# Kernel tuning notes

Measured on AMD Instinct MI355X. Metric: run time of the kernel, lower is better.

The kernel has to match this reference:

```python
import jax, jax.numpy as jnp
import numpy as np

NUM_SITES = 64
BOND_DIM = 64
PHYS_DIM = 2
BATCH = 8192
INIT_STD = 0.125  # 1/sqrt(bond_dim)
EPS_AMP = 1e-12
EPS_LOG = 1e-30


def setup_inputs() -> dict:
    key = jax.random.key(0)
    k_cfg, k_l, k_b, k_r = jax.random.split(key, 4)
    configurations = jax.random.randint(k_cfg, (BATCH, NUM_SITES), 0, PHYS_DIM, dtype=jnp.int32)
    left = jax.random.normal(k_l, (PHYS_DIM, BOND_DIM), dtype=jnp.float32) * INIT_STD
    bulk = jax.random.normal(k_b, (NUM_SITES - 2, BOND_DIM, PHYS_DIM, BOND_DIM), dtype=jnp.float32) * INIT_STD
    right = jax.random.normal(k_r, (BOND_DIM, PHYS_DIM), dtype=jnp.float32) * INIT_STD
    return {"configurations": configurations, "left": left, "bulk": bulk, "right": right}


def _psi(configurations, left, bulk, right):
    # configurations: [B, S] int; left: [d, D]; bulk: [S-2, D, d, D]; right: [D, d]
    B = configurations.shape[0]
    env0 = left[configurations[:, 0]]  # [B, D]
    cfg_mid = configurations[:, 1:-1].T  # [S-2, B]

    def step(env, xs):
        site_t, idx = xs  # site_t: [D, d, D], idx: [B]
        D = site_t.shape[0]
        # env @ site (contract left bond), then gather the per-sample physical slice
        tmp = (env @ site_t.reshape(D, -1)).reshape(B, PHYS_DIM, D)  # [B, d, D]
        env = jnp.take_along_axis(tmp, idx[:, None, None], axis=1)[:, 0, :]  # [B, D]
        return env, None

    env, _ = jax.lax.scan(step, env0, (bulk, cfg_mid))
    cols = jnp.take(right, configurations[:, -1], axis=1).T  # [B, D]
    return jnp.sum(env * cols, axis=1)  # [B]


def _log_norm(left, bulk, right):
    env0 = left.T @ left  # [D, D]  (real dtype -> conj trivial)

    def step(carry, site_t):
        env, log_scale = carry
        sm = jnp.transpose(site_t, (1, 0, 2))  # [d, D, D]
        env = jnp.einsum('pdi,de,pej->ij', sm, env, sm)  # sum_p A_p^H env A_p
        scale = jnp.maximum(jnp.max(jnp.abs(env)), EPS_LOG)
        return (env / scale, log_scale + jnp.log(scale)), None

    (env, log_scale), _ = jax.lax.scan(step, (env0, jnp.zeros((), left.dtype)), bulk)
    z = jnp.sum(right * (env @ right))
    return jnp.log(jnp.maximum(z, EPS_LOG)) + log_scale


def reference(configurations, left, bulk, right):
    psi = _psi(configurations, left, bulk, right)
    abs_sq = jnp.maximum(psi * psi, EPS_AMP)
    log_z = _log_norm(left, bulk, right)
    nll = -(jnp.log(abs_sq) - log_z)
    return jnp.mean(nll)
```

## Files before the change

kernel.cpp:

```cpp
#include <hip/hip_runtime.h>
#include <math.h>

#define NBULK 62
#define SB    72

typedef __attribute__((ext_vector_type(8))) short bf8_t;
typedef __attribute__((ext_vector_type(4))) float f4_t;

#define MFMA(a, b, c) __builtin_amdgcn_mfma_f32_16x16x32_bf16((a), (b), (c), 0, 0, 0)

__device__ __forceinline__ unsigned short f2bf(float f) {
    unsigned int u = __float_as_uint(f);
    return (unsigned short)((u + 0x7FFFu + ((u >> 16) & 1u)) >> 16);
}
__device__ __forceinline__ float bf2f(unsigned short h) {
    return __uint_as_float(((unsigned int)h) << 16);
}

__device__ __forceinline__ void gload16(const void* g, void* l) {
    __builtin_amdgcn_global_load_lds(
        (const __attribute__((address_space(1))) unsigned int*)g,
        (__attribute__((address_space(3))) unsigned int*)l, 16, 0, 0);
}

#define WS_E_OFF   1024
#define WS_B_OFF   6144
#define WS_BT_OFF  45056
#define WS_MR_OFF  1060864


extern "C" __global__ __launch_bounds__(256)
void mps_precompute(const float* __restrict__ bulkG,
                    unsigned short* __restrict__ BTg,
                    unsigned short* __restrict__ MRg)
{
    __shared__ unsigned short BTl[8192];
    __shared__ unsigned short MRl[8192];
    const int s = blockIdx.x, tid = threadIdx.x;
    const float4* src = (const float4*)(bulkG + (size_t)s * 8192);
    for (int c = 0; c < 8; ++c) {
        int idx = tid + c * 256;
        float4 v = src[idx];
        int f  = idx * 4;
        int kk = f >> 7;
        int p  = (f >> 6) & 1;
        int j  = f & 63;
        unsigned short b0 = f2bf(v.x), b1 = f2bf(v.y), b2 = f2bf(v.z), b3 = f2bf(v.w);
        int n = p * 64 + kk;
        int off = n * 64 + (((j >> 3) ^ (n & 7)) << 3) + (j & 7);
        MRl[off + 0] = b0; MRl[off + 1] = b1; MRl[off + 2] = b2; MRl[off + 3] = b3;
        unsigned short bb[4] = {b0, b1, b2, b3};
        #pragma unroll
        for (int t2 = 0; t2 < 4; ++t2) {
            int n2 = p * 64 + j + t2;
            BTl[n2 * 64 + (((kk >> 3) ^ (n2 & 7)) << 3) + (kk & 7)] = bb[t2];
        }
    }
    __syncthreads();
    const uint4* bt4 = (const uint4*)BTl;
    const uint4* mr4 = (const uint4*)MRl;
    uint4* btg = (uint4*)(BTg + (size_t)s * 8192);
    uint4* mrg = (uint4*)(MRg + (size_t)s * 8192);
    for (int c = 0; c < 4; ++c) {
        int idx = tid + c * 256;
        btg[idx] = bt4[idx];
        mrg[idx] = mr4[idx];
    }
}

extern "C" __global__ __launch_bounds__(256)
void mps_main(const int* __restrict__ cfgG, const float* __restrict__ leftG,
              const float* __restrict__ rightG, float* __restrict__ wsF,
              const unsigned short* __restrict__ BTg,
              const unsigned short* __restrict__ MRg)
{
    extern __shared__ char smem[];
    unsigned short* smem16 = (unsigned short*)smem;
    const int tid  = threadIdx.x;
    const int bid  = blockIdx.x;
    const int wv   = tid >> 6;
    const int lane = tid & 63;
    const int quad = lane >> 4;
    const int ln   = lane & 15;

    if (bid >= 2) {
        unsigned short* Bb0  = smem16;
        unsigned short* Bb1  = Bb0 + 8192;
        unsigned short* env  = Bb1 + 8192;
        unsigned char*  selT = (unsigned char*)(env + 64 * SB);

        const int s0 = (bid - 2) * 64;
        {
            int m = tid >> 2, part = tid & 3;
            const int* row = cfgG + (size_t)(s0 + m) * 64 + part * 16;
            #pragma unroll
            for (int q = 0; q < 4; ++q) {
                int4 v = *(const int4*)(row + q * 4);
                int cb = part * 16 + q * 4;
                selT[(cb + 0) * 64 + m] = (unsigned char)v.x;
                selT[(cb + 1) * 64 + m] = (unsigned char)v.y;
                selT[(cb + 2) * 64 + m] = (unsigned char)v.z;
                selT[(cb + 3) * 64 + m] = (unsigned char)v.w;
            }
        }
        {
            const char* g0 = (const char*)BTg;
            for (int c = 0; c < 4; ++c) {
                int chunk = wv * 4 + c;
                gload16(g0 + chunk * 1024 + (size_t)lane * 16, (char*)Bb0 + chunk * 1024);
            }
        }
        __syncthreads();

        bf8_t Af[2];
        {
            int sel0 = selT[0 * 64 + wv * 16 + ln];
            const float* lp0 = leftG + sel0 * 64;
            #pragma unroll
            for (int h = 0; h < 2; ++h) {
                float4 a = *(const float4*)(lp0 + h * 32 + quad * 8);
                float4 b = *(const float4*)(lp0 + h * 32 + quad * 8 + 4);
                bf8_t t;
                t[0] = (short)f2bf(a.x); t[1] = (short)f2bf(a.y);
                t[2] = (short)f2bf(a.z); t[3] = (short)f2bf(a.w);
                t[4] = (short)f2bf(b.x); t[5] = (short)f2bf(b.y);
                t[6] = (short)f2bf(b.z); t[7] = (short)f2bf(b.w);
                Af[h] = t;
            }
        }

        for (int t = 0; t < NBULK; ++t) {
            __syncthreads();
            unsigned short* B = (t & 1) ? Bb1 : Bb0;
            if (t + 1 < NBULK) {
                const char* gn = (const char*)(BTg + (size_t)(t + 1) * 8192);
                char* l = (char*)((t & 1) ? Bb0 : Bb1);
                for (int c = 0; c < 4; ++c) {
                    int chunk = wv * 4 + c;
                    gload16(gn + chunk * 1024 + (size_t)lane * 16, l + chunk * 1024);
                }
            }
            bf8_t Bf[2][4][2];
            #pragma unroll
            for (int b2 = 0; b2 < 2; ++b2)
                #pragma unroll
                for (int ct = 0; ct < 4; ++ct) {
                    int row = b2 * 64 + ct * 16 + ln;
                    #pragma unroll
                    for (int h = 0; h < 2; ++h)
                        Bf[b2][ct][h] = *(const bf8_t*)(B + row * 64 + (((h * 4 + quad) ^ (ln & 7)) << 3));
                }
            f4_t acc[2][4];
            #pragma unroll
            for (int b2 = 0; b2 < 2; ++b2)
                #pragma unroll
                for (int ct = 0; ct < 4; ++ct) {
                    f4_t a = {0.f, 0.f, 0.f, 0.f};
                    a = MFMA(Af[0], Bf[b2][ct][0], a);
                    a = MFMA(Af[1], Bf[b2][ct][1], a);
                    acc[b2][ct] = a;
                }
            unsigned int sv = *(const unsigned int*)(selT + (t + 1) * 64 + wv * 16 + quad * 4);
            #pragma unroll
            for (int ct = 0; ct < 4; ++ct)
                #pragma unroll
                for (int r = 0; r < 4; ++r) {
                    float v = ((sv >> (8 * r)) & 1u) ? acc[1][ct][r] : acc[0][ct][r];
                    env[(wv * 16 + quad * 4 + r) * SB + ct * 16 + ln] = f2bf(v);
                }
            Af[0] = *(const bf8_t*)(env + (wv * 16 + ln) * SB + quad * 8);
            Af[1] = *(const bf8_t*)(env + (wv * 16 + ln) * SB + 32 + quad * 8);
        }
        {
            int selL = selT[63 * 64 + wv * 16 + ln];
            bf8_t e0 = *(const bf8_t*)(env + (wv * 16 + ln) * SB + quad * 16);
            bf8_t e1 = *(const bf8_t*)(env + (wv * 16 + ln) * SB + quad * 16 + 8);
            float p = 0.f;
            #pragma unroll
            for (int j = 0; j < 8; ++j)
                p = fmaf(bf2f((unsigned short)e0[j]), rightG[(quad * 16 + j) * 2 + selL], p);
            #pragma unroll
            for (int j = 0; j < 8; ++j)
                p = fmaf(bf2f((unsigned short)e1[j]), rightG[(quad * 16 + 8 + j) * 2 + selL], p);
            p += __shfl_xor(p, 16);
            p += __shfl_xor(p, 32);
            float lp = logf(fmaxf(p * p, 1e-12f));
            lp += __shfl_xor(lp, 1); lp += __shfl_xor(lp, 2);
            lp += __shfl_xor(lp, 4); lp += __shfl_xor(lp, 8);
            if (lane == 0) atomicAdd(&wsF[0], lp);
        }
    } else {
        unsigned short* Ebf = smem16;
        unsigned short* St0 = Ebf + 64 * SB;
        unsigned short* St1 = St0 + 64 * SB;
        unsigned short* Ms0 = St1 + 64 * SB;
        unsigned short* Ms1 = Ms0 + 8192;
        float* wred = (float*)(Ms1 + 8192);

        const bool fwd = (bid == 0);
        const unsigned short* srcbase = fwd ? BTg : MRg;
        {
            int i = tid >> 2, jq = tid & 3;
            for (int jj = 0; jj < 16; ++jj) {
                int j = jq * 16 + jj;
                float v;
                if (fwd) v = leftG[i] * leftG[j] + leftG[64 + i] * leftG[64 + j];
                else     v = rightG[i * 2] * rightG[j * 2] + rightG[i * 2 + 1] * rightG[j * 2 + 1];
                Ebf[i * SB + j] = f2bf(v);
            }
        }
        {
            int st = fwd ? 0 : 61;
            const char* g = (const char*)(srcbase + (size_t)st * 8192);
            for (int c = 0; c < 4; ++c) {
                int chunk = wv * 4 + c;
                gload16(g + chunk * 1024 + (size_t)lane * 16, (char*)Ms0 + chunk * 1024);
            }
        }
        float lsum = 0.f;
        const int p   = wv >> 1;
        const int ntb = (wv & 1) * 2;
        const int mta = (wv >> 1) * 2;
        const int nta = (wv & 1) * 2;
        unsigned short* Stp = p ? St1 : St0;

        for (int k = 0; k < 31; ++k) {
            __syncthreads();
            unsigned short* M = (k & 1) ? Ms1 : Ms0;
            if (k + 1 < 31) {
                int sn = fwd ? (k + 1) : (61 - (k + 1));
                const char* g = (const char*)(srcbase + (size_t)sn * 8192);
                char* l = (char*)((k & 1) ? Ms0 : Ms1);
                for (int c = 0; c < 4; ++c) {
                    int chunk = wv * 4 + c;
                    gload16(g + chunk * 1024 + (size_t)lane * 16, l + chunk * 1024);
                }
            }
            float inv = 1.f;
            if (k > 0) {
                const float* wp = wred + ((k - 1) & 1) * 4;
                float mm = fmaxf(fmaxf(wp[0], wp[1]), fmaxf(wp[2], wp[3]));
                float sc = fmaxf(mm, 1e-30f);
                inv = 1.f / sc;
                if (tid == 0) lsum += logf(sc);
            }
            {
                bf8_t Af2[4][2];
                #pragma unroll
                for (int mt = 0; mt < 4; ++mt)
                    #pragma unroll
                    for (int h = 0; h < 2; ++h)
                        Af2[mt][h] = *(const bf8_t*)(Ebf + (mt * 16 + ln) * SB + h * 32 + quad * 8);
                #pragma unroll
                for (int c = 0; c < 2; ++c) {
                    int nt = ntb + c;
                    int row = p * 64 + nt * 16 + ln;
                    bf8_t B0 = *(const bf8_t*)(M + row * 64 + (((0 + quad) ^ (ln & 7)) << 3));
                    bf8_t B1 = *(const bf8_t*)(M + row * 64 + (((4 + quad) ^ (ln & 7)) << 3));
                    #pragma unroll
                    for (int mt = 0; mt < 4; ++mt) {
                        f4_t a = {0.f, 0.f, 0.f, 0.f};
                        a = MFMA(Af2[mt][0], B0, a);
                        a = MFMA(Af2[mt][1], B1, a);
                        ushort4 pk;
                        pk.x = f2bf(a[0]); pk.y = f2bf(a[1]); pk.z = f2bf(a[2]); pk.w = f2bf(a[3]);
                        *(ushort4*)(Stp + (nt * 16 + ln) * SB + mt * 16 + quad * 4) = pk;
                    }
                }
            }
            __syncthreads();
            {
                bf8_t Aw[2][2][2], Bw[2][2][2];
                #pragma unroll
                for (int pp = 0; pp < 2; ++pp)
                    #pragma unroll
                    for (int mi = 0; mi < 2; ++mi)
                        #pragma unroll
                        for (int h = 0; h < 2; ++h)
                            Aw[pp][mi][h] = *(const bf8_t*)(M + (pp * 64 + (mta + mi) * 16 + ln) * 64
                                                              + (((h * 4 + quad) ^ (ln & 7)) << 3));
                #pragma unroll
                for (int pp = 0; pp < 2; ++pp)
                    #pragma unroll
                    for (int ni = 0; ni < 2; ++ni)
                        #pragma unroll
                        for (int h = 0; h < 2; ++h)
                            Bw[pp][ni][h] = *(const bf8_t*)((pp ? St1 : St0)
                                                            + ((nta + ni) * 16 + ln) * SB + h * 32 + quad * 8);
                float mx = 0.f;
                #pragma unroll
                for (int mi = 0; mi < 2; ++mi)
                    #pragma unroll
                    for (int ni = 0; ni < 2; ++ni) {
                        f4_t a = {0.f, 0.f, 0.f, 0.f};
                        #pragma unroll
                        for (int pp = 0; pp < 2; ++pp)
                            #pragma unroll
                            for (int h = 0; h < 2; ++h)
                                a = MFMA(Aw[pp][mi][h], Bw[pp][ni][h], a);
                        #pragma unroll
                        for (int r = 0; r < 4; ++r) {
                            float val = a[r] * inv;
                            mx = fmaxf(mx, fabsf(val));
                            Ebf[((mta + mi) * 16 + quad * 4 + r) * SB + (nta + ni) * 16 + ln] = f2bf(val);
                        }
                    }
                #pragma unroll
                for (int off = 32; off > 0; off >>= 1)
                    mx = fmaxf(mx, __shfl_xor(mx, off));
                if (lane == 0) wred[(k & 1) * 4 + wv] = mx;
            }
        }
        __syncthreads();
        float* dst = wsF + (fwd ? WS_E_OFF : WS_B_OFF);
        for (int c = 0; c < 16; ++c) {
            int idx = tid + c * 256;
            dst[idx] = bf2f(Ebf[(idx >> 6) * SB + (idx & 63)]);
        }
        if (tid == 0) wsF[fwd ? 1 : 2] = lsum;
    }
}

extern "C" __global__ void mps_finalize(const float* __restrict__ wsF, float* __restrict__ out)
{
    const int lane = threadIdx.x;
    const float* E  = wsF + WS_E_OFF;
    const float* Bm = wsF + WS_B_OFF;
    float a = 0.f;
    #pragma unroll 8
    for (int j = 0; j < 64; ++j)
        a = fmaf(E[lane * 64 + j], Bm[lane * 64 + j], a);
    #pragma unroll
    for (int off = 32; off > 0; off >>= 1)
        a += __shfl_down(a, off);
    if (lane == 0) {
        const float z = fmaxf(a, 1e-30f);
        const float log_z = logf(z) + wsF[1] + wsF[2];
        out[0] = log_z - wsF[0] * (1.0f / 8192.0f);
    }
}

extern "C" void kernel_launch(void* const* d_in, const int* in_sizes, int n_in,
                              void* d_out, int out_size, void* d_ws, size_t ws_size,
                              hipStream_t stream)
{
    const int*   cfg   = (const int*)d_in[0];
    const float* left  = (const float*)d_in[1];
    const float* bulk  = (const float*)d_in[2];
    const float* right = (const float*)d_in[3];
    float* wsF = (float*)d_ws;
    unsigned short* BTg = (unsigned short*)((char*)d_ws + WS_BT_OFF);
    unsigned short* MRg = (unsigned short*)((char*)d_ws + WS_MR_OFF);

    hipMemsetAsync(d_ws, 0, 16, stream);
    mps_precompute<<<dim3(62), dim3(256), 0, stream>>>(bulk, BTg, MRg);
    mps_main<<<dim3(130), dim3(256), 60480, stream>>>(cfg, left, right, wsF, BTg, MRg);
    mps_finalize<<<dim3(1), dim3(64), 0, stream>>>(wsF, (float*)d_out);
}
```

Measured before the change: 119.4 us.

## Fuse finalize into main kernel, drop memset, bit-pack configs, swizzle LDS layouts

Removes the memset and the separate finalize launch. Workspace zeroing moves into the precompute kernel, and the last block to finish (detected with an atomic counter) computes the final reduction. The psi path now packs each sample's configuration into a 64-bit register instead of an LDS byte table, and swaps the MFMA operand roles so each lane writes and reads its own env row with an XOR swizzle. The norm path moves to a swizzled 64-wide layout with a cheaper lgkmcnt barrier. Together these cut launch overhead and LDS padding, but the last-block pattern depends on the atomic and fence ordering being correct.

```diff
diff --git a/kernel.cpp b/kernel.cpp
--- a/kernel.cpp
+++ b/kernel.cpp
@@ -2,12 +2,13 @@
 #include <math.h>
 
 #define NBULK 62
-#define SB    72
+#define NBLK  130
 
 typedef __attribute__((ext_vector_type(8))) short bf8_t;
 typedef __attribute__((ext_vector_type(4))) float f4_t;
 
 #define MFMA(a, b, c) __builtin_amdgcn_mfma_f32_16x16x32_bf16((a), (b), (c), 0, 0, 0)
+#define LGKM_BARRIER() asm volatile("s_waitcnt lgkmcnt(0)\n\ts_barrier" ::: "memory")
 
 __device__ __forceinline__ unsigned short f2bf(float f) {
     unsigned int u = __float_as_uint(f);
@@ -16,7 +17,6 @@
 __device__ __forceinline__ float bf2f(unsigned short h) {
     return __uint_as_float(((unsigned int)h) << 16);
 }
-
 __device__ __forceinline__ void gload16(const void* g, void* l) {
     __builtin_amdgcn_global_load_lds(
         (const __attribute__((address_space(1))) unsigned int*)g,
@@ -28,15 +28,19 @@
 #define WS_BT_OFF  45056
 #define WS_MR_OFF  1060864
 
-
 extern "C" __global__ __launch_bounds__(256)
 void mps_precompute(const float* __restrict__ bulkG,
                     unsigned short* __restrict__ BTg,
-                    unsigned short* __restrict__ MRg)
+                    unsigned short* __restrict__ MRg,
+                    float* __restrict__ wsF)
 {
     __shared__ unsigned short BTl[8192];
     __shared__ unsigned short MRl[8192];
     const int s = blockIdx.x, tid = threadIdx.x;
+    if (s == 0 && tid == 0) {
+        wsF[0] = 0.f; wsF[1] = 0.f; wsF[2] = 0.f;
+        ((int*)wsF)[3] = 0;
+    }
     const float4* src = (const float4*)(bulkG + (size_t)s * 8192);
     for (int c = 0; c < 8; ++c) {
         int idx = tid + c * 256;
@@ -68,11 +72,12 @@
     }
 }
 
-extern "C" __global__ __launch_bounds__(256)
+extern "C" __global__ __launch_bounds__(256, 1)
 void mps_main(const int* __restrict__ cfgG, const float* __restrict__ leftG,
               const float* __restrict__ rightG, float* __restrict__ wsF,
               const unsigned short* __restrict__ BTg,
-              const unsigned short* __restrict__ MRg)
+              const unsigned short* __restrict__ MRg,
+              float* __restrict__ outG)
 {
     extern __shared__ char smem[];
     unsigned short* smem16 = (unsigned short*)smem;
@@ -82,106 +87,103 @@
     const int lane = tid & 63;
     const int quad = lane >> 4;
     const int ln   = lane & 15;
+    const int swz  = ln & 7;
 
     if (bid >= 2) {
-        unsigned short* Bb0  = smem16;
-        unsigned short* Bb1  = Bb0 + 8192;
-        unsigned short* env  = Bb1 + 8192;
-        unsigned char*  selT = (unsigned char*)(env + 64 * SB);
-
-        const int s0 = (bid - 2) * 64;
-        {
-            int m = tid >> 2, part = tid & 3;
-            const int* row = cfgG + (size_t)(s0 + m) * 64 + part * 16;
-            #pragma unroll
-            for (int q = 0; q < 4; ++q) {
+        unsigned short* Tb0 = smem16;
+        unsigned short* Tb1 = Tb0 + 8192;
+        unsigned short* env = Tb1 + 8192;
+
+        const int s0  = (bid - 2) * 64;
+        const int sMy = wv * 16 + ln;
+        const int esw = (sMy & 7) << 3;
+        unsigned short* eb = env + sMy * 64;
+
+        unsigned long long SEL = 0ull;
+        {
+            const int* row = cfgG + (size_t)(s0 + sMy) * 64;
+            #pragma unroll
+            for (int q = 0; q < 16; ++q) {
                 int4 v = *(const int4*)(row + q * 4);
-                int cb = part * 16 + q * 4;
-                selT[(cb + 0) * 64 + m] = (unsigned char)v.x;
-                selT[(cb + 1) * 64 + m] = (unsigned char)v.y;
-                selT[(cb + 2) * 64 + m] = (unsigned char)v.z;
-                selT[(cb + 3) * 64 + m] = (unsigned char)v.w;
+                SEL |= ((unsigned long long)(v.x & 1)) << (q * 4);
+                SEL |= ((unsigned long long)(v.y & 1)) << (q * 4 + 1);
+                SEL |= ((unsigned long long)(v.z & 1)) << (q * 4 + 2);
+                SEL |= ((unsigned long long)(v.w & 1)) << (q * 4 + 3);
             }
         }
         {
             const char* g0 = (const char*)BTg;
             for (int c = 0; c < 4; ++c) {
                 int chunk = wv * 4 + c;
-                gload16(g0 + chunk * 1024 + (size_t)lane * 16, (char*)Bb0 + chunk * 1024);
-            }
-        }
-        __syncthreads();
-
-        bf8_t Af[2];
-        {
-            int sel0 = selT[0 * 64 + wv * 16 + ln];
-            const float* lp0 = leftG + sel0 * 64;
-            #pragma unroll
-            for (int h = 0; h < 2; ++h) {
-                float4 a = *(const float4*)(lp0 + h * 32 + quad * 8);
-                float4 b = *(const float4*)(lp0 + h * 32 + quad * 8 + 4);
-                bf8_t t;
-                t[0] = (short)f2bf(a.x); t[1] = (short)f2bf(a.y);
-                t[2] = (short)f2bf(a.z); t[3] = (short)f2bf(a.w);
-                t[4] = (short)f2bf(b.x); t[5] = (short)f2bf(b.y);
-                t[6] = (short)f2bf(b.z); t[7] = (short)f2bf(b.w);
-                Af[h] = t;
-            }
+                gload16(g0 + chunk * 1024 + (size_t)lane * 16, (char*)Tb0 + chunk * 1024);
+            }
+        }
+        bf8_t Ef0, Ef1;
+        {
+            int sel0 = (int)(SEL & 1ull);
+            const float* lp = leftG + sel0 * 64;
+            bf8_t t0, t1;
+            #pragma unroll
+            for (int j = 0; j < 8; ++j) {
+                t0[j] = (short)f2bf(lp[quad * 8 + j]);
+                t1[j] = (short)f2bf(lp[32 + quad * 8 + j]);
+            }
+            Ef0 = t0; Ef1 = t1;
         }
 
         for (int t = 0; t < NBULK; ++t) {
             __syncthreads();
-            unsigned short* B = (t & 1) ? Bb1 : Bb0;
+            unsigned short* Tl = (t & 1) ? Tb1 : Tb0;
             if (t + 1 < NBULK) {
                 const char* gn = (const char*)(BTg + (size_t)(t + 1) * 8192);
-                char* l = (char*)((t & 1) ? Bb0 : Bb1);
+                char* l = (char*)((t & 1) ? Tb0 : Tb1);
                 for (int c = 0; c < 4; ++c) {
                     int chunk = wv * 4 + c;
                     gload16(gn + chunk * 1024 + (size_t)lane * 16, l + chunk * 1024);
                 }
             }
-            bf8_t Bf[2][4][2];
-            #pragma unroll
-            for (int b2 = 0; b2 < 2; ++b2)
-                #pragma unroll
-                for (int ct = 0; ct < 4; ++ct) {
-                    int row = b2 * 64 + ct * 16 + ln;
-                    #pragma unroll
-                    for (int h = 0; h < 2; ++h)
-                        Bf[b2][ct][h] = *(const bf8_t*)(B + row * 64 + (((h * 4 + quad) ^ (ln & 7)) << 3));
-                }
-            f4_t acc[2][4];
-            #pragma unroll
-            for (int b2 = 0; b2 < 2; ++b2)
-                #pragma unroll
-                for (int ct = 0; ct < 4; ++ct) {
-                    f4_t a = {0.f, 0.f, 0.f, 0.f};
-                    a = MFMA(Af[0], Bf[b2][ct][0], a);
-                    a = MFMA(Af[1], Bf[b2][ct][1], a);
-                    acc[b2][ct] = a;
-                }
-            unsigned int sv = *(const unsigned int*)(selT + (t + 1) * 64 + wv * 16 + quad * 4);
-            #pragma unroll
-            for (int ct = 0; ct < 4; ++ct)
-                #pragma unroll
-                for (int r = 0; r < 4; ++r) {
-                    float v = ((sv >> (8 * r)) & 1u) ? acc[1][ct][r] : acc[0][ct][r];
-                    env[(wv * 16 + quad * 4 + r) * SB + ct * 16 + ln] = f2bf(v);
-                }
-            Af[0] = *(const bf8_t*)(env + (wv * 16 + ln) * SB + quad * 8);
-            Af[1] = *(const bf8_t*)(env + (wv * 16 + ln) * SB + 32 + quad * 8);
-        }
-        {
-            int selL = selT[63 * 64 + wv * 16 + ln];
-            bf8_t e0 = *(const bf8_t*)(env + (wv * 16 + ln) * SB + quad * 16);
-            bf8_t e1 = *(const bf8_t*)(env + (wv * 16 + ln) * SB + quad * 16 + 8);
+            f4_t a0[4], a1[4];
+            #pragma unroll
+            for (int mt = 0; mt < 4; ++mt) {
+                const unsigned short* r0 = Tl + (mt * 16 + ln) * 64;
+                const unsigned short* r1 = Tl + (64 + mt * 16 + ln) * 64;
+                bf8_t A00 = *(const bf8_t*)(r0 + ((quad       ^ swz) << 3));
+                bf8_t A01 = *(const bf8_t*)(r0 + (((4 + quad) ^ swz) << 3));
+                bf8_t A10 = *(const bf8_t*)(r1 + ((quad       ^ swz) << 3));
+                bf8_t A11 = *(const bf8_t*)(r1 + (((4 + quad) ^ swz) << 3));
+                f4_t x = {0.f, 0.f, 0.f, 0.f};
+                x = MFMA(A00, Ef0, x);
+                x = MFMA(A01, Ef1, x);
+                a0[mt] = x;
+                f4_t y = {0.f, 0.f, 0.f, 0.f};
+                y = MFMA(A10, Ef0, y);
+                y = MFMA(A11, Ef1, y);
+                a1[mt] = y;
+            }
+            const bool bs = ((SEL >> (t + 1)) & 1ull) != 0ull;
+            #pragma unroll
+            for (int mt = 0; mt < 4; ++mt) {
+                ushort4 pk;
+                pk.x = f2bf(bs ? a1[mt][0] : a0[mt][0]);
+                pk.y = f2bf(bs ? a1[mt][1] : a0[mt][1]);
+                pk.z = f2bf(bs ? a1[mt][2] : a0[mt][2]);
+                pk.w = f2bf(bs ? a1[mt][3] : a0[mt][3]);
+                *(ushort4*)(eb + ((mt * 16 + quad * 4) ^ esw)) = pk;
+            }
+            Ef0 = *(const bf8_t*)(eb + ((quad * 8)      ^ esw));
+            Ef1 = *(const bf8_t*)(eb + ((quad * 8 + 32) ^ esw));
+        }
+        {
+            const int selL = (int)((SEL >> 63) & 1ull);
             float p = 0.f;
             #pragma unroll
-            for (int j = 0; j < 8; ++j)
-                p = fmaf(bf2f((unsigned short)e0[j]), rightG[(quad * 16 + j) * 2 + selL], p);
-            #pragma unroll
-            for (int j = 0; j < 8; ++j)
-                p = fmaf(bf2f((unsigned short)e1[j]), rightG[(quad * 16 + 8 + j) * 2 + selL], p);
+            for (int g2 = 0; g2 < 2; ++g2) {
+                int g = quad * 2 + g2;
+                bf8_t e = *(const bf8_t*)(eb + ((g * 8) ^ esw));
+                #pragma unroll
+                for (int j = 0; j < 8; ++j)
+                    p = fmaf(bf2f((unsigned short)e[j]), rightG[(g * 8 + j) * 2 + selL], p);
+            }
             p += __shfl_xor(p, 16);
             p += __shfl_xor(p, 32);
             float lp = logf(fmaxf(p * p, 1e-12f));
@@ -190,12 +192,11 @@
             if (lane == 0) atomicAdd(&wsF[0], lp);
         }
     } else {
-        unsigned short* Ebf = smem16;
-        unsigned short* St0 = Ebf + 64 * SB;
-        unsigned short* St1 = St0 + 64 * SB;
-        unsigned short* Ms0 = St1 + 64 * SB;
-        unsigned short* Ms1 = Ms0 + 8192;
-        float* wred = (float*)(Ms1 + 8192);
+        unsigned short* Tb0 = smem16;
+        unsigned short* Tb1 = Tb0 + 8192;
+        unsigned short* E   = Tb1 + 8192;
+        unsigned short* St  = E + 4096;
+        float* wred = (float*)(St + 8192);
 
         const bool fwd = (bid == 0);
         const unsigned short* srcbase = fwd ? BTg : MRg;
@@ -206,7 +207,7 @@
                 float v;
                 if (fwd) v = leftG[i] * leftG[j] + leftG[64 + i] * leftG[64 + j];
                 else     v = rightG[i * 2] * rightG[j * 2] + rightG[i * 2 + 1] * rightG[j * 2 + 1];
-                Ebf[i * SB + j] = f2bf(v);
+                E[i * 64 + (j ^ ((i & 7) << 3))] = f2bf(v);
             }
         }
         {
@@ -214,7 +215,7 @@
             const char* g = (const char*)(srcbase + (size_t)st * 8192);
             for (int c = 0; c < 4; ++c) {
                 int chunk = wv * 4 + c;
-                gload16(g + chunk * 1024 + (size_t)lane * 16, (char*)Ms0 + chunk * 1024);
+                gload16(g + chunk * 1024 + (size_t)lane * 16, (char*)Tb0 + chunk * 1024);
             }
         }
         float lsum = 0.f;
@@ -222,15 +223,14 @@
         const int ntb = (wv & 1) * 2;
         const int mta = (wv >> 1) * 2;
         const int nta = (wv & 1) * 2;
-        unsigned short* Stp = p ? St1 : St0;
 
         for (int k = 0; k < 31; ++k) {
             __syncthreads();
-            unsigned short* M = (k & 1) ? Ms1 : Ms0;
+            unsigned short* Tl = (k & 1) ? Tb1 : Tb0;
             if (k + 1 < 31) {
                 int sn = fwd ? (k + 1) : (61 - (k + 1));
                 const char* g = (const char*)(srcbase + (size_t)sn * 8192);
-                char* l = (char*)((k & 1) ? Ms0 : Ms1);
+                char* l = (char*)((k & 1) ? Tb0 : Tb1);
                 for (int c = 0; c < 4; ++c) {
                     int chunk = wv * 4 + c;
                     gload16(g + chunk * 1024 + (size_t)lane * 16, l + chunk * 1024);
@@ -245,69 +245,68 @@
                 if (tid == 0) lsum += logf(sc);
             }
             {
-                bf8_t Af2[4][2];
-                #pragma unroll
-                for (int mt = 0; mt < 4; ++mt)
+                bf8_t Bf[2][2];
+                #pragma unroll
+                for (int c = 0; c < 2; ++c) {
+                    const unsigned short* rb = Tl + (p * 64 + (ntb + c) * 16 + ln) * 64;
+                    Bf[c][0] = *(const bf8_t*)(rb + ((quad       ^ swz) << 3));
+                    Bf[c][1] = *(const bf8_t*)(rb + (((4 + quad) ^ swz) << 3));
+                }
+                #pragma unroll
+                for (int it = 0; it < 4; ++it) {
+                    const unsigned short* er = E + (it * 16 + ln) * 64;
+                    bf8_t A0 = *(const bf8_t*)(er + ((quad * 8)      ^ (swz << 3)));
+                    bf8_t A1 = *(const bf8_t*)(er + ((quad * 8 + 32) ^ (swz << 3)));
                     #pragma unroll
-                    for (int h = 0; h < 2; ++h)
-                        Af2[mt][h] = *(const bf8_t*)(Ebf + (mt * 16 + ln) * SB + h * 32 + quad * 8);
-                #pragma unroll
-                for (int c = 0; c < 2; ++c) {
-                    int nt = ntb + c;
-                    int row = p * 64 + nt * 16 + ln;
-                    bf8_t B0 = *(const bf8_t*)(M + row * 64 + (((0 + quad) ^ (ln & 7)) << 3));
-                    bf8_t B1 = *(const bf8_t*)(M + row * 64 + (((4 + quad) ^ (ln & 7)) << 3));
-                    #pragma unroll
-                    for (int mt = 0; mt < 4; ++mt) {
-                        f4_t a = {0.f, 0.f, 0.f, 0.f};
-                        a = MFMA(Af2[mt][0], B0, a);
-                        a = MFMA(Af2[mt][1], B1, a);
+                    for (int c = 0; c < 2; ++c) {
+                        f4_t x = {0.f, 0.f, 0.f, 0.f};
+                        x = MFMA(A0, Bf[c][0], x);
+                        x = MFMA(A1, Bf[c][1], x);
+                        int n = (ntb + c) * 16 + ln;
                         ushort4 pk;
-                        pk.x = f2bf(a[0]); pk.y = f2bf(a[1]); pk.z = f2bf(a[2]); pk.w = f2bf(a[3]);
-                        *(ushort4*)(Stp + (nt * 16 + ln) * SB + mt * 16 + quad * 4) = pk;
+                        pk.x = f2bf(x[0]); pk.y = f2bf(x[1]); pk.z = f2bf(x[2]); pk.w = f2bf(x[3]);
+                        *(ushort4*)(St + p * 4096 + n * 64 + ((it * 16 + quad * 4) ^ ((n & 7) << 3))) = pk;
                     }
                 }
             }
-            __syncthreads();
+            LGKM_BARRIER();
             {
-                bf8_t Aw[2][2][2], Bw[2][2][2];
-                #pragma unroll
-                for (int pp = 0; pp < 2; ++pp)
-                    #pragma unroll
-                    for (int mi = 0; mi < 2; ++mi)
-                        #pragma unroll
-                        for (int h = 0; h < 2; ++h)
-                            Aw[pp][mi][h] = *(const bf8_t*)(M + (pp * 64 + (mta + mi) * 16 + ln) * 64
-                                                              + (((h * 4 + quad) ^ (ln & 7)) << 3));
-                #pragma unroll
-                for (int pp = 0; pp < 2; ++pp)
-                    #pragma unroll
-                    for (int ni = 0; ni < 2; ++ni)
-                        #pragma unroll
-                        for (int h = 0; h < 2; ++h)
-                            Bw[pp][ni][h] = *(const bf8_t*)((pp ? St1 : St0)
-                                                            + ((nta + ni) * 16 + ln) * SB + h * 32 + quad * 8);
-                float mx = 0.f;
+                f4_t o[2][2];
                 #pragma unroll
                 for (int mi = 0; mi < 2; ++mi)
                     #pragma unroll
                     for (int ni = 0; ni < 2; ++ni) {
-                        f4_t a = {0.f, 0.f, 0.f, 0.f};
+                        f4_t x = {0.f, 0.f, 0.f, 0.f};
                         #pragma unroll
-                        for (int pp = 0; pp < 2; ++pp)
-                            #pragma unroll
-                            for (int h = 0; h < 2; ++h)
-                                a = MFMA(Aw[pp][mi][h], Bw[pp][ni][h], a);
-                        #pragma unroll
-                        for (int r = 0; r < 4; ++r) {
-                            float val = a[r] * inv;
-                            mx = fmaxf(mx, fabsf(val));
-                            Ebf[((mta + mi) * 16 + quad * 4 + r) * SB + (nta + ni) * 16 + ln] = f2bf(val);
+                        for (int pp = 0; pp < 2; ++pp) {
+                            const unsigned short* ar = Tl + (pp * 64 + (mta + mi) * 16 + ln) * 64;
+                            bf8_t A0 = *(const bf8_t*)(ar + ((quad       ^ swz) << 3));
+                            bf8_t A1 = *(const bf8_t*)(ar + (((4 + quad) ^ swz) << 3));
+                            int n2 = (nta + ni) * 16 + ln;
+                            const unsigned short* br = St + pp * 4096 + n2 * 64;
+                            bf8_t B0 = *(const bf8_t*)(br + ((quad * 8)      ^ ((n2 & 7) << 3)));
+                            bf8_t B1 = *(const bf8_t*)(br + ((quad * 8 + 32) ^ ((n2 & 7) << 3)));
+                            x = MFMA(A0, B0, x);
+                            x = MFMA(A1, B1, x);
                         }
+                        o[mi][ni] = x;
                     }
-                #pragma unroll
-                for (int off = 32; off > 0; off >>= 1)
-                    mx = fmaxf(mx, __shfl_xor(mx, off));
+                float mx = 0.f;
+                #pragma unroll
+                for (int mi = 0; mi < 2; ++mi)
+                    #pragma unroll
+                    for (int ni = 0; ni < 2; ++ni) {
+                        float v0 = o[mi][ni][0] * inv, v1 = o[mi][ni][1] * inv;
+                        float v2 = o[mi][ni][2] * inv, v3 = o[mi][ni][3] * inv;
+                        mx = fmaxf(mx, fmaxf(fmaxf(fabsf(v0), fabsf(v1)), fmaxf(fabsf(v2), fabsf(v3))));
+                        ushort4 pk;
+                        pk.x = f2bf(v0); pk.y = f2bf(v1); pk.z = f2bf(v2); pk.w = f2bf(v3);
+                        int n2 = (nta + ni) * 16 + ln;
+                        *(ushort4*)(E + n2 * 64 + (((mta + mi) * 16 + quad * 4) ^ ((n2 & 7) << 3))) = pk;
+                    }
+                mx = fmaxf(mx, __shfl_xor(mx, 1));  mx = fmaxf(mx, __shfl_xor(mx, 2));
+                mx = fmaxf(mx, __shfl_xor(mx, 4));  mx = fmaxf(mx, __shfl_xor(mx, 8));
+                mx = fmaxf(mx, __shfl_xor(mx, 16)); mx = fmaxf(mx, __shfl_xor(mx, 32));
                 if (lane == 0) wred[(k & 1) * 4 + wv] = mx;
             }
         }
@@ -315,28 +314,43 @@
         float* dst = wsF + (fwd ? WS_E_OFF : WS_B_OFF);
         for (int c = 0; c < 16; ++c) {
             int idx = tid + c * 256;
-            dst[idx] = bf2f(Ebf[(idx >> 6) * SB + (idx & 63)]);
+            int i = idx >> 6, j = idx & 63;
+            dst[idx] = bf2f(E[i * 64 + (j ^ ((i & 7) << 3))]);
         }
         if (tid == 0) wsF[fwd ? 1 : 2] = lsum;
     }
-}
-
-extern "C" __global__ void mps_finalize(const float* __restrict__ wsF, float* __restrict__ out)
-{
-    const int lane = threadIdx.x;
-    const float* E  = wsF + WS_E_OFF;
-    const float* Bm = wsF + WS_B_OFF;
-    float a = 0.f;
-    #pragma unroll 8
-    for (int j = 0; j < 64; ++j)
-        a = fmaf(E[lane * 64 + j], Bm[lane * 64 + j], a);
-    #pragma unroll
-    for (int off = 32; off > 0; off >>= 1)
-        a += __shfl_down(a, off);
-    if (lane == 0) {
-        const float z = fmaxf(a, 1e-30f);
-        const float log_z = logf(z) + wsF[1] + wsF[2];
-        out[0] = log_z - wsF[0] * (1.0f / 8192.0f);
+
+    __syncthreads();
+    __threadfence();
+    __syncthreads();
+    int* eflag = (int*)smem;
+    if (tid == 0) {
+        int old = atomicAdd((int*)wsF + 3, 1);
+        eflag[0] = (old == NBLK - 1) ? 1 : 0;
+    }
+    __syncthreads();
+    if (eflag[0]) {
+        __threadfence();
+        const float4* Ew = (const float4*)(wsF + WS_E_OFF);
+        const float4* Bw = (const float4*)(wsF + WS_B_OFF);
+        float a = 0.f;
+        #pragma unroll
+        for (int c = 0; c < 4; ++c) {
+            int idx = tid + c * 256;
+            float4 e = Ew[idx], b = Bw[idx];
+            a += e.x * b.x + e.y * b.y + e.z * b.z + e.w * b.w;
+        }
+        #pragma unroll
+        for (int off = 32; off > 0; off >>= 1)
+            a += __shfl_down(a, off);
+        float* ered = (float*)smem + 8;
+        if ((tid & 63) == 0) ered[tid >> 6] = a;
+        __syncthreads();
+        if (tid == 0) {
+            float z = fmaxf(ered[0] + ered[1] + ered[2] + ered[3], 1e-30f);
+            float log_z = logf(z) + wsF[1] + wsF[2];
+            outG[0] = log_z - wsF[0] * (1.0f / 8192.0f);
+        }
     }
 }
 
@@ -352,8 +366,6 @@
     unsigned short* BTg = (unsigned short*)((char*)d_ws + WS_BT_OFF);
     unsigned short* MRg = (unsigned short*)((char*)d_ws + WS_MR_OFF);
 
-    hipMemsetAsync(d_ws, 0, 16, stream);
-    mps_precompute<<<dim3(62), dim3(256), 0, stream>>>(bulk, BTg, MRg);
-    mps_main<<<dim3(130), dim3(256), 60480, stream>>>(cfg, left, right, wsF, BTg, MRg);
-    mps_finalize<<<dim3(1), dim3(64), 0, stream>>>(wsF, (float*)d_out);
-}
+    mps_precompute<<<dim3(62), dim3(256), 0, stream>>>(bulk, BTg, MRg, wsF);
+    mps_main<<<dim3(NBLK), dim3(256), 57472, stream>>>(cfg, left, right, wsF, BTg, MRg, (float*)d_out);
+}
```

Result: no change. 120.5 us (+0.9%).
